# Kernel optimization log

Measured on AMD Instinct MI355X. Metric: run time of the kernel, lower is better.

Reference implementation:

```python
import jax, jax.numpy as jnp
import numpy as np
from jax import lax

SEQ_LENGTH = 32
B, I, O = 1024, 2048, 1024
DT = 1e-3
TAU_PRE, TAU_POST = 0.02, 0.02
ETA_PLUS, ETA_MINUS = 1e-3, 1e-3
W_MIN, W_MAX = -1.0, 1.0
TAU_MEM = 0.02
V_TH = 1.0


def setup_inputs() -> dict:
    key = jax.random.key(0)
    k1, k2, k3 = jax.random.split(key, 3)
    # Bernoulli(0.05) input spikes, rate-coded, reused each timestep
    input_spikes = (jax.random.uniform(k1, (B, I)) < 0.05).astype(jnp.float32)
    weight = jax.random.normal(k2, (O, I), dtype=jnp.float32) * (1.0 / np.sqrt(I))
    bias = jax.random.normal(k3, (O,), dtype=jnp.float32) * 0.01
    return {"input_spikes": input_spikes, "weight": weight, "bias": bias}


def reference(input_spikes, weight, bias):
    decay_pre = jnp.exp(jnp.float32(-DT / TAU_PRE))
    decay_post = jnp.exp(jnp.float32(-DT / TAU_POST))
    v_decay = jnp.exp(jnp.float32(-DT / TAU_MEM))

    b = input_spikes.shape[0]
    v0 = jnp.zeros((b, O), dtype=input_spikes.dtype)
    z0 = jnp.zeros((b, O), dtype=input_spikes.dtype)
    # STDPState(t_pre=1.0, t_post=1.0) broadcast to trace shapes
    tpre0 = jnp.ones((b, I), dtype=input_spikes.dtype)
    tpost0 = jnp.ones((b, O), dtype=input_spikes.dtype)

    def step(carry, _):
        v, w, tpre, tpost, _z = carry
        # linear projection with current (plastic) weights
        z_in = input_spikes @ w.T + bias  # [B, O]
        # LIF output neuron: decay, integrate, threshold, reset
        v = v * v_decay + z_in
        z_out = (v >= V_TH).astype(v.dtype)
        v = v * (1.0 - z_out)
        # STDP trace update: decay then accumulate spikes
        tpre = tpre * decay_pre + input_spikes
        tpost = tpost * decay_post + z_out
        # spike-gated eligibility outer products, summed over batch
        dw = (ETA_PLUS * jnp.einsum('bo,bi->oi', z_out, tpre)
              - ETA_MINUS * jnp.einsum('bo,bi->oi', tpost, input_spikes))
        w = jnp.clip(w + dw, W_MIN, W_MAX)
        return (v, w, tpre, tpost, z_out), None

    (v, w, tpre, tpost, z_out), _ = lax.scan(
        step, (v0, weight, tpre0, tpost0, z0), None, length=SEQ_LENGTH)
    return z_out, v, w
```

## Files before the change

kernel.cpp:

```cpp
#include <hip/hip_runtime.h>
#include <cmath>

#define SEQ 32
#define BB 1024
#define II 2048
#define OO 1024

typedef unsigned short ushortt;

__global__ void build_idx_rev(const float* __restrict__ x, ushortt* __restrict__ idxArr,
                              int* __restrict__ cntArr, int* __restrict__ rcnt,
                              ushortt* __restrict__ rev, ushortt* __restrict__ idxT) {
  int b = blockIdx.x;
  int lane = threadIdx.x;
  __shared__ ushortt sIdx[256];
  const float* row = x + (long)b * II;
  int base = 0;
  for (int c = 0; c < II / 64; ++c) {
    float val = row[c * 64 + lane];
    unsigned long long m = __ballot(val != 0.0f);
    if (val != 0.0f) {
      int pos = base + __popcll(m & ((1ull << lane) - 1ull));
      if (pos < 256) {
        idxArr[(b << 8) + pos] = (ushortt)(c * 64 + lane);
        sIdx[pos] = (ushortt)(c * 64 + lane);
      }
    }
    base += __popcll(m);
  }
  int cnt = base < 256 ? base : 256;
  if (lane == 0) cntArr[b] = cnt;
  __syncthreads();
  {
    int j0 = lane * 4;
    ushort4 u;
    u.x = (j0 + 0 < cnt) ? sIdx[j0 + 0] : (ushortt)II;
    u.y = (j0 + 1 < cnt) ? sIdx[j0 + 1] : (ushortt)II;
    u.z = (j0 + 2 < cnt) ? sIdx[j0 + 2] : (ushortt)II;
    u.w = (j0 + 3 < cnt) ? sIdx[j0 + 3] : (ushortt)II;
    ((ushort4*)idxT)[(lane << 10) + b] = u;
  }
  for (int j = lane; j < cnt; j += 64) {
    int i = sIdx[j];
    int pos = atomicAdd(&rcnt[i], 1);
    if (pos < 128) rev[((long)i << 7) + pos] = (ushortt)b;
  }
}

__global__ void transpose2_f32(const float* __restrict__ zC, const float* __restrict__ vC,
                               float* __restrict__ oz, float* __restrict__ ov) {
  __shared__ float t[32][33];
  const float* src = blockIdx.z ? vC : zC;
  float* dst = blockIdx.z ? ov : oz;
  int c0 = blockIdx.x * 32, r0 = blockIdx.y * 32;
  int tx = threadIdx.x, ty = threadIdx.y;
#pragma unroll
  for (int k = 0; k < 4; k++)
    t[ty + k * 8][tx] = src[(long)(r0 + ty + k * 8) * BB + c0 + tx];
  __syncthreads();
#pragma unroll
  for (int k = 0; k < 4; k++)
    dst[(long)(c0 + ty + k * 8) * OO + r0 + tx] = t[tx][ty + k * 8];
}

__global__ __launch_bounds__(512, 8) void snn_kernel(
    const float* __restrict__ w, const float* __restrict__ bias,
    const ushortt* __restrict__ idxT, const int* __restrict__ cntArr,
    const int* __restrict__ rcnt, const ushortt* __restrict__ rev,
    const ushortt* __restrict__ idxArr,
    float* __restrict__ zC, float* __restrict__ vC, float* __restrict__ outw,
    float dec) {
  int o = blockIdx.x, tid = threadIdx.x, lane = tid & 63, wave = tid >> 6;
  __shared__ float shbuf[9219];
  __shared__ int sCnt, sFlag, cFlag;
  float* wL = shbuf;
  float* aG = shbuf + 2049;
  float* nG = shbuf + 4098;
  float* mL = shbuf + 6147;
  int* sList = (int*)(shbuf + 8195);
  float* Sfix = shbuf + 6147;
  float* SnuD = shbuf + 7171;
  float* SAD = shbuf + 8195;

#pragma unroll
  for (int q = 0; q < 4; ++q) {
    int i = q * 512 + tid;
    wL[i] = w[(long)o * II + i];
    aG[i] = 0.f;
    nG[i] = (float)rcnt[i];
  }
#pragma unroll
  for (int k = 0; k < 2; ++k) {
    int b = k * 512 + tid;
    Sfix[b] = 0.f; SnuD[b] = 0.f; SAD[b] = 0.f;
  }
  if (tid == 0) {
    sFlag = 0; cFlag = 0;
    wL[II] = 0.f; aG[II] = 0.f; nG[II] = 0.f;
  }

  int jmax[2];
#pragma unroll
  for (int k = 0; k < 2; ++k) {
    int c = cntArr[k * 512 + wave * 64 + lane];
#pragma unroll
    for (int off = 32; off > 0; off >>= 1) c = max(c, __shfl_xor(c, off));
    jmax[k] = c;
  }
  float bo = bias[o];
  unsigned clipped = 0;
  bool everSpk = false;
  float p = 1.f, u = 1.f;
  __syncthreads();

  const ushort4* tpb = (const ushort4*)idxT;
  double S[2];
  float Snu[2], SA[2], v4[2], zk[2];
#pragma unroll
  for (int k = 0; k < 2; ++k) {
    int b = k * 512 + tid;
    double s = 0.0;
    float sn = 0.f;
    int jm4 = (jmax[k] + 3) >> 2;
    const ushort4* tp = tpb + b;
    ushort4 nx = tp[0];
    for (int g = 0; g < jm4; ++g) {
      ushort4 u0 = nx;
      nx = tp[((g + 1) << 10)];
      int a_ = u0.x, b_ = u0.y, c_ = u0.z, d_ = u0.w;
      s += (double)wL[a_]; s += (double)wL[b_]; s += (double)wL[c_]; s += (double)wL[d_];
      sn += nG[a_]; sn += nG[b_]; sn += nG[c_]; sn += nG[d_];
    }
    S[k] = s; Snu[k] = sn;
    SA[k] = 0.f; v4[k] = 0.f; zk[k] = 0.f;
  }

  for (int t = 0; t < SEQ; ++t) {
    p *= dec; u *= dec; u += 1.f;
    float spre = u - p;
    int local = 0;
#pragma unroll
    for (int k = 0; k < 2; ++k) {
      float zin = (float)S[k] + bo;
      float nv = v4[k] * dec + zin;
      float z = (nv >= 1.f) ? 1.f : 0.f;
      nv = nv * (1.f - z);
      v4[k] = nv; zk[k] = z;
      if (z != 0.f) local = 1;
    }
    if (local) sFlag = 1;
    __syncthreads();
    int spk = sFlag;

    if (!spk) {
#pragma unroll
      for (int q = 0; q < 4; ++q) {
        int i = q * 512 + tid;
        bool already = (clipped >> q) & 1u;
        float n = 0.f, atn = 0.f, fix = 0.f;
        bool cl = false;
        if (!already) {
          n = nG[i];
          atn = everSpk ? (dec * aG[i]) : 0.f;
          float dw = -(1e-3f * (p * n + atn));
          float wold = wL[i];
          float pre = wold + dw;
          float wv = fminf(fmaxf(pre, -1.f), 1.f);
          cl = (pre <= -1.f);
          if (cl) {
            clipped |= 1u << q;
            fix = (-1.f - wold) - dw;
            nG[i] = 0.f;
            if (everSpk) aG[i] = 0.f;
          } else if (everSpk) {
            aG[i] = atn;
          }
          wL[i] = wv;
        }
        unsigned long long m = __ballot(cl);
        if (m) {
          if (lane == 0) cFlag = 1;
          while (m) {
            int src = __builtin_ctzll(m);
            m &= m - 1;
            int ii = __shfl(i, src);
            float fx = __shfl(fix, src);
            float mn = -__shfl(n, src);
            float ma = -__shfl(atn, src);
            int rc = rcnt[ii];
            const ushortt* rp = rev + ((long)ii << 7);
            for (int r = lane; r < rc; r += 64) {
              int b2 = rp[r];
              atomicAdd(&Sfix[b2], fx);
              atomicAdd(&SnuD[b2], mn);
              if (everSpk) atomicAdd(&SAD[b2], ma);
            }
          }
        }
      }
      __syncthreads();
      float coefP = 1e-3f * p;
      if (cFlag) {
#pragma unroll
        for (int k = 0; k < 2; ++k) {
          int b = k * 512 + tid;
          S[k] = S[k] - (double)coefP * (double)Snu[k]
                      - (double)1e-3f * (double)(dec * SA[k])
                      + (double)Sfix[b];
          SA[k] = dec * SA[k] + SAD[b];
          Snu[k] = Snu[k] + SnuD[b];
          Sfix[b] = 0.f; SnuD[b] = 0.f; SAD[b] = 0.f;
        }
      } else {
#pragma unroll
        for (int k = 0; k < 2; ++k) {
          S[k] = S[k] - (double)coefP * (double)Snu[k]
                      - (double)1e-3f * (double)(dec * SA[k]);
          SA[k] = dec * SA[k];
        }
      }
      if (tid == 0) { sFlag = 0; cFlag = 0; }
      __syncthreads();
    } else {
      everSpk = true;
      if (tid == 0) sCnt = 0;
      __syncthreads();
#pragma unroll
      for (int k = 0; k < 2; ++k)
        if (zk[k] != 0.f) { int pos = atomicAdd(&sCnt, 1); sList[pos] = k * 512 + tid; }
#pragma unroll
      for (int q = 0; q < 4; ++q) mL[q * 512 + tid] = 0.f;
      __syncthreads();
      int ns = sCnt;
      for (int s = wave; s < ns; s += 8) {
        int b = sList[s];
        int cb = cntArr[b];
        const ushortt* ip = idxArr + (b << 8);
        for (int j = lane; j < cb; j += 64)
          atomicAdd(&mL[ip[j]], 1.f);
      }
      __syncthreads();
      float cv = (float)ns;
#pragma unroll
      for (int q = 0; q < 4; ++q) {
        int i = q * 512 + tid;
        float mt = mL[i];
        float atn = dec * aG[i] + mt;
        float n = (float)rcnt[i];
        float dw = 1e-3f * (p * cv + spre * mt) - 1e-3f * (p * n + atn);
        float wold = wL[i];
        float pre = wold + dw;
        float wv = fminf(fmaxf(pre, -1.f), 1.f);
        bool cl = (pre <= -1.f);
        if (cl) clipped |= 1u << q; else clipped &= ~(1u << q);
        wL[i] = wv;
        aG[i] = cl ? 0.f : atn;
        nG[i] = cl ? 0.f : n;
      }
      __syncthreads();
#pragma unroll
      for (int k = 0; k < 2; ++k) {
        int b = k * 512 + tid;
        double s = 0.0;
        float sa = 0.f, sn = 0.f;
        int jm4 = (jmax[k] + 3) >> 2;
        const ushort4* tp = tpb + b;
        ushort4 nx = tp[0];
        for (int g = 0; g < jm4; ++g) {
          ushort4 u0 = nx;
          nx = tp[((g + 1) << 10)];
          int a_ = u0.x, b_ = u0.y, c_ = u0.z, d_ = u0.w;
          s += (double)wL[a_]; sa += aG[a_]; sn += nG[a_];
          s += (double)wL[b_]; sa += aG[b_]; sn += nG[b_];
          s += (double)wL[c_]; sa += aG[c_]; sn += nG[c_];
          s += (double)wL[d_]; sa += aG[d_]; sn += nG[d_];
        }
        S[k] = s; SA[k] = sa; Snu[k] = sn;
      }
#pragma unroll
      for (int k = 0; k < 2; ++k) {
        int b = k * 512 + tid;
        Sfix[b] = 0.f; SnuD[b] = 0.f; SAD[b] = 0.f;
      }
      if (tid == 0) { sFlag = 0; cFlag = 0; }
      __syncthreads();
    }
  }

  __syncthreads();
#pragma unroll
  for (int q = 0; q < 4; ++q) outw[(long)o * II + q * 512 + tid] = wL[q * 512 + tid];
#pragma unroll
  for (int k = 0; k < 2; ++k) {
    int b = k * 512 + tid;
    zC[(long)o * BB + b] = zk[k];
    vC[(long)o * BB + b] = v4[k];
  }
}

extern "C" void kernel_launch(void* const* d_in, const int* in_sizes, int n_in,
                              void* d_out, int out_size, void* d_ws, size_t ws_size,
                              hipStream_t stream) {
  const float* x = (const float*)d_in[0];
  const float* w = (const float*)d_in[1];
  const float* bias = (const float*)d_in[2];
  float* out = (float*)d_out;

  char* ws = (char*)d_ws;
  ushortt* idxArr = (ushortt*)(ws + 0);
  int* cntArr = (int*)(ws + 524288);
  ushortt* idxT = (ushortt*)(ws + 528384);
  int* rcnt = (int*)(ws + 1060864);
  ushortt* rev = (ushortt*)(ws + 1069056);
  float* zC = (float*)(ws + 1593344);
  float* vC = (float*)(ws + 5787648);

  hipMemsetAsync(rcnt, 0, II * sizeof(int), stream);
  build_idx_rev<<<BB, 64, 0, stream>>>(x, idxArr, cntArr, rcnt, rev, idxT);

  const float dec = (float)exp(-0.05);

  snn_kernel<<<OO, 512, 0, stream>>>(w, bias, idxT, cntArr, rcnt, rev, idxArr,
                                     zC, vC, out + 2 * BB * OO, dec);

  transpose2_f32<<<dim3(BB / 32, OO / 32, 2), dim3(32, 8), 0, stream>>>(zC, vC, out, out + BB * OO);
}
```

Baseline: 287.6 us.

## Drop shared nG array, track clip-flip deltas incrementally to cut LDS

Removes the per-input nG shared array and reads rcnt from global in the non-spike path instead. In the spike path, Snu is no longer recomputed by gathering over nG; it is patched with per-batch deltas pushed via atomics for inputs whose clip state changed. Shared memory is aliased more tightly and the manual index prefetch in gather loops is dropped. This cuts LDS footprint, which may allow more resident blocks, and removes gather work, at the cost of extra global reads and atomic scatter when clip states flip.

```diff
diff --git a/kernel.cpp b/kernel.cpp
--- a/kernel.cpp
+++ b/kernel.cpp
@@ -71,32 +71,29 @@
     float* __restrict__ zC, float* __restrict__ vC, float* __restrict__ outw,
     float dec) {
   int o = blockIdx.x, tid = threadIdx.x, lane = tid & 63, wave = tid >> 6;
-  __shared__ float shbuf[9219];
+  __shared__ float shbuf[8195];
   __shared__ int sCnt, sFlag, cFlag;
   float* wL = shbuf;
   float* aG = shbuf + 2049;
-  float* nG = shbuf + 4098;
-  float* mL = shbuf + 6147;
-  int* sList = (int*)(shbuf + 8195);
-  float* Sfix = shbuf + 6147;
+  float* mL = shbuf + 4098;
+  int* sList = (int*)(shbuf + 6147);
   float* SnuD = shbuf + 7171;
-  float* SAD = shbuf + 8195;
+  float* nT = shbuf + 4098;
+  float* Sfix = shbuf + 4098;
+  float* SAD = shbuf + 6147;
 
 #pragma unroll
   for (int q = 0; q < 4; ++q) {
     int i = q * 512 + tid;
     wL[i] = w[(long)o * II + i];
     aG[i] = 0.f;
-    nG[i] = (float)rcnt[i];
-  }
-#pragma unroll
-  for (int k = 0; k < 2; ++k) {
-    int b = k * 512 + tid;
-    Sfix[b] = 0.f; SnuD[b] = 0.f; SAD[b] = 0.f;
-  }
+    nT[i] = (float)rcnt[i];
+  }
+#pragma unroll
+  for (int k = 0; k < 2; ++k) SnuD[k * 512 + tid] = 0.f;
   if (tid == 0) {
     sFlag = 0; cFlag = 0;
-    wL[II] = 0.f; aG[II] = 0.f; nG[II] = 0.f;
+    wL[II] = 0.f; aG[II] = 0.f; nT[II] = 0.f;
   }
 
   int jmax[2];
@@ -123,16 +120,20 @@
     float sn = 0.f;
     int jm4 = (jmax[k] + 3) >> 2;
     const ushort4* tp = tpb + b;
-    ushort4 nx = tp[0];
     for (int g = 0; g < jm4; ++g) {
-      ushort4 u0 = nx;
-      nx = tp[((g + 1) << 10)];
+      ushort4 u0 = tp[(g << 10)];
       int a_ = u0.x, b_ = u0.y, c_ = u0.z, d_ = u0.w;
       s += (double)wL[a_]; s += (double)wL[b_]; s += (double)wL[c_]; s += (double)wL[d_];
-      sn += nG[a_]; sn += nG[b_]; sn += nG[c_]; sn += nG[d_];
+      sn += nT[a_]; sn += nT[b_]; sn += nT[c_]; sn += nT[d_];
     }
     S[k] = s; Snu[k] = sn;
     SA[k] = 0.f; v4[k] = 0.f; zk[k] = 0.f;
+  }
+  __syncthreads();
+#pragma unroll
+  for (int k = 0; k < 2; ++k) {
+    int b = k * 512 + tid;
+    Sfix[b] = 0.f; SAD[b] = 0.f;
   }
 
   for (int t = 0; t < SEQ; ++t) {
@@ -160,7 +161,7 @@
         float n = 0.f, atn = 0.f, fix = 0.f;
         bool cl = false;
         if (!already) {
-          n = nG[i];
+          n = (float)rcnt[i];
           atn = everSpk ? (dec * aG[i]) : 0.f;
           float dw = -(1e-3f * (p * n + atn));
           float wold = wL[i];
@@ -170,7 +171,6 @@
           if (cl) {
             clipped |= 1u << q;
             fix = (-1.f - wold) - dw;
-            nG[i] = 0.f;
             if (everSpk) aG[i] = 0.f;
           } else if (everSpk) {
             aG[i] = atn;
@@ -252,35 +252,44 @@
         float pre = wold + dw;
         float wv = fminf(fmaxf(pre, -1.f), 1.f);
         bool cl = (pre <= -1.f);
+        bool was = (clipped >> q) & 1u;
         if (cl) clipped |= 1u << q; else clipped &= ~(1u << q);
         wL[i] = wv;
         aG[i] = cl ? 0.f : atn;
-        nG[i] = cl ? 0.f : n;
+        bool flip = (cl != was);
+        float dn = cl ? -n : n;
+        unsigned long long m = __ballot(flip);
+        while (m) {
+          int src = __builtin_ctzll(m);
+          m &= m - 1;
+          int ii = __shfl(i, src);
+          float d = __shfl(dn, src);
+          int rc = rcnt[ii];
+          const ushortt* rp = rev + ((long)ii << 7);
+          for (int r = lane; r < rc; r += 64)
+            atomicAdd(&SnuD[rp[r]], d);
+        }
       }
       __syncthreads();
 #pragma unroll
       for (int k = 0; k < 2; ++k) {
         int b = k * 512 + tid;
         double s = 0.0;
-        float sa = 0.f, sn = 0.f;
+        float sa = 0.f;
         int jm4 = (jmax[k] + 3) >> 2;
         const ushort4* tp = tpb + b;
-        ushort4 nx = tp[0];
         for (int g = 0; g < jm4; ++g) {
-          ushort4 u0 = nx;
-          nx = tp[((g + 1) << 10)];
+          ushort4 u0 = tp[(g << 10)];
           int a_ = u0.x, b_ = u0.y, c_ = u0.z, d_ = u0.w;
-          s += (double)wL[a_]; sa += aG[a_]; sn += nG[a_];
-          s += (double)wL[b_]; sa += aG[b_]; sn += nG[b_];
-          s += (double)wL[c_]; sa += aG[c_]; sn += nG[c_];
-          s += (double)wL[d_]; sa += aG[d_]; sn += nG[d_];
-        }
-        S[k] = s; SA[k] = sa; Snu[k] = sn;
-      }
-#pragma unroll
-      for (int k = 0; k < 2; ++k) {
-        int b = k * 512 + tid;
-        Sfix[b] = 0.f; SnuD[b] = 0.f; SAD[b] = 0.f;
+          s += (double)wL[a_]; sa += aG[a_];
+          s += (double)wL[b_]; sa += aG[b_];
+          s += (double)wL[c_]; sa += aG[c_];
+          s += (double)wL[d_]; sa += aG[d_];
+        }
+        S[k] = s; SA[k] = sa;
+        Snu[k] = Snu[k] + SnuD[b];
+        SnuD[b] = 0.f;
+        Sfix[b] = 0.f; SAD[b] = 0.f;
       }
       if (tid == 0) { sFlag = 0; cFlag = 0; }
       __syncthreads();
```

After: 276.9 us. 1.04x faster.
